# Optimization experiments

Hardware: AMD Instinct MI355X
Metric: run time of the kernel (lower is better)

Reference implementation:

```python
import jax, jax.numpy as jnp
import numpy as np

B, C, H, W = 256, 3, 128, 128
K = 16                      # vae_small.img_size == kernel == stride (non-overlapping)
GH, GW = H // K, W // K
P = C * K * K               # 768 flattened patch dim
HID = 2048
L = 256                     # latent_size


def setup_inputs() -> dict:
    key = jax.random.key(0)
    ks = jax.random.split(key, 9)
    s = 0.02
    f32 = jnp.float32
    return {
        "x": jax.random.uniform(ks[0], (B, C, H, W), f32),
        "w_enc1": jax.random.normal(ks[1], (P, HID), f32) * s,
        "b_enc1": jnp.zeros((HID,), f32),
        "w_enc2": jax.random.normal(ks[2], (HID, 2 * L), f32) * s,
        "b_enc2": jnp.zeros((2 * L,), f32),
        "w_dec1": jax.random.normal(ks[3], (L, HID), f32) * s,
        "b_dec1": jnp.zeros((HID,), f32),
        "w_dec2": jax.random.normal(ks[4], (HID, P), f32) * s,
        "b_dec2": jnp.zeros((P,), f32),
    }


def reference(x, w_enc1, b_enc1, w_enc2, b_enc2, w_dec1, b_dec1, w_dec2, b_dec2):
    b, c, h, w = x.shape
    gh, gw = h // K, w // K
    # unfold: [b,c,h,w] -> [b,gh,gw, c*K*K]  (same padding is 0 when stride==k)
    patches = (x.reshape(b, c, gh, K, gw, K)
                .transpose(0, 2, 4, 1, 3, 5)
                .reshape(b, gh, gw, c * K * K))
    # batched per-patch VAE encode (replaces the python map/unbind loop)
    he = jax.nn.relu(patches @ w_enc1 + b_enc1)            # [b,gh,gw,HID]
    mu_logvar = he @ w_enc2 + b_enc2                        # [b,gh,gw,2L]
    mu = mu_logvar[..., :L]
    z = mu                                                  # deterministic reparameterize
    # batched per-patch decode
    hd = jax.nn.relu(z @ w_dec1 + b_dec1)                   # [b,gh,gw,HID]
    dec = jax.nn.sigmoid(hd @ w_dec2 + b_dec2)              # [b,gh,gw,P]
    # fold: exact inverse of unfold since stride == kernel
    recon_x = (dec.reshape(b, gh, gw, c, K, K)
                 .transpose(0, 3, 1, 4, 2, 5)
                 .reshape(b, c, h, w))
    mu_logvar_2d = jnp.transpose(mu_logvar, (0, 3, 1, 2))   # [b, 2L, gh, gw]
    return recon_x, mu_logvar_2d
```

## Files before the change

### kernel.cpp

```cpp
#include <hip/hip_runtime.h>
#include <hip/hip_bf16.h>
#include <stdint.h>

typedef __bf16 bf16x8_t __attribute__((ext_vector_type(8)));
typedef float f32x4_t __attribute__((ext_vector_type(4)));
typedef unsigned short ushort8_t __attribute__((ext_vector_type(8)));

__device__ __forceinline__ unsigned short f2bf(float f) {
    union { float f; uint32_t i; } v; v.f = f;
    uint32_t i = v.i + (((v.i >> 16) & 1u) + 0x7FFFu);
    return (unsigned short)(i >> 16);
}

typedef const __attribute__((address_space(1))) void* gas_t;
typedef __attribute__((address_space(3))) void* las_t;
__device__ __forceinline__ void load_lds16(const unsigned short* g, unsigned short* l) {
    __builtin_amdgcn_global_load_lds((gas_t)g, (las_t)l, 16, 0, 0);
}

#define BB   256
#define CC   3
#define HH   128
#define WW   128
#define PP   768
#define HID  2048
#define LL   256
#define MM   16384

__global__ void patchify(const float* __restrict__ x,
                         unsigned short* __restrict__ patches) {
    int t = blockIdx.x * 256 + threadIdx.x;
    int e = t * 8;
    int col = e & 127;
    int row = (e >> 7) & 127;
    int c   = (e >> 14) % 3;
    int b   = e / (128 * 128 * 3);
    int gh = row >> 4, kh = row & 15, gw = col >> 4, kw = col & 15;
    long po = (long)(b * 64 + gh * 8 + gw) * PP + c * 256 + kh * 16 + kw;
    float4 v0 = *(const float4*)(x + e);
    float4 v1 = *(const float4*)(x + e + 4);
    ushort8_t o;
    o[0] = f2bf(v0.x); o[1] = f2bf(v0.y); o[2] = f2bf(v0.z); o[3] = f2bf(v0.w);
    o[4] = f2bf(v1.x); o[5] = f2bf(v1.y); o[6] = f2bf(v1.z); o[7] = f2bf(v1.w);
    *(ushort8_t*)(patches + po) = o;
}

__global__ void transpose_k(const float* __restrict__ in,
                            unsigned short* __restrict__ out, int R, int C) {
    __shared__ unsigned short tile[32][34];
    int nbc = C >> 5;
    int tc = blockIdx.x % nbc, tr = blockIdx.x / nbc;
    int tx = threadIdx.x & 31, ty0 = threadIdx.x >> 5;
    int r0 = tr << 5, c0 = tc << 5;
    #pragma unroll
    for (int i = 0; i < 4; ++i) {
        int ty = ty0 + i * 8;
        tile[ty][tx] = f2bf(in[(long)(r0 + ty) * C + c0 + tx]);
    }
    __syncthreads();
    #pragma unroll
    for (int i = 0; i < 4; ++i) {
        int ty = ty0 + i * 8;
        out[(long)(c0 + ty) * R + r0 + tx] = tile[tx][ty];
    }
}

#define BMT 256
#define BNT 128
#define BKT 32
#define LDS_TILE ((BMT + BNT) * BKT)

template <int ACT, int WMODE>
__global__ void __launch_bounds__(512, 4)
gemm_bt(const unsigned short* __restrict__ A, int lda,
        const unsigned short* __restrict__ Bt,
        const float* __restrict__ bias,
        unsigned short* __restrict__ C0u,
        float* __restrict__ C0f,
        float* __restrict__ C1f,
        int ldc, int Kd, int nbn, int m0) {
    __shared__ __align__(16) unsigned short lds_buf[3 * LDS_TILE];
    const int nbm = gridDim.x / nbn;
    const int stripe = nbm >> 3;
    const int xcd = blockIdx.x & 7;
    const int loc = blockIdx.x >> 3;
    const int bm = xcd * stripe + (loc % stripe);
    const int bn = loc / stripe;
    const int tid = threadIdx.x;
    const int wave = tid >> 6;
    const int lane = tid & 63;
    const int wr = wave >> 1;
    const int wc = wave & 1;
    const int fr = lane & 15;
    const int quad = lane >> 4;

    const int Gl = tid ^ ((tid >> 3) & 7);
    const int sr = Gl >> 2;
    const int sg = (Gl & 3) << 3;

    const unsigned short* Ab = A + (long)bm * BMT * lda;
    const unsigned short* Bb = Bt + (long)bn * BNT * Kd;

    int gA[4], gB[4];
    #pragma unroll
    for (int i = 0; i < 4; ++i) {
        const int r = (wr << 6) + (i << 4) + fr;
        gA[i] = ((((r << 2) | quad) ^ ((r >> 1) & 7)) << 3);
    }
    #pragma unroll
    for (int j = 0; j < 4; ++j) {
        const int r = (wc << 6) + (j << 4) + fr;
        gB[j] = ((((r << 2) | quad) ^ ((r >> 1) & 7)) << 3);
    }

    f32x4_t acc[4][4];
    #pragma unroll
    for (int i = 0; i < 4; ++i)
        #pragma unroll
        for (int j = 0; j < 4; ++j)
            acc[i][j] = (f32x4_t){0.f, 0.f, 0.f, 0.f};

    const int nt = Kd / BKT;

    #define STAGE(t, buf) do {                                                 \
        unsigned short* Al_ = (buf);                                           \
        unsigned short* Bl_ = Al_ + BMT * BKT;                                 \
        const long k0_ = (long)(t) * BKT;                                      \
        load_lds16(Ab + (long)sr * lda + k0_ + sg,         Al_ + (wave << 9)); \
        load_lds16(Ab + (long)(sr + 128) * lda + k0_ + sg,                     \
                   Al_ + 4096 + (wave << 9));                                  \
        load_lds16(Bb + (long)sr * Kd + k0_ + sg,          Bl_ + (wave << 9)); \
    } while (0)

    STAGE(0, lds_buf);
    STAGE(1, lds_buf + LDS_TILE);
    asm volatile("s_waitcnt vmcnt(3)" ::: "memory");
    __builtin_amdgcn_s_barrier();
    __builtin_amdgcn_sched_barrier(0);

    int rb = 0;
    int sbx = 2;
    for (int t = 0; t < nt; ++t) {
        if (t + 2 < nt) STAGE(t + 2, lds_buf + sbx * LDS_TILE);
        const unsigned short* Al = lds_buf + rb * LDS_TILE;
        const unsigned short* Bl = Al + BMT * BKT;
        bf16x8_t af[4], bfr[4];
        #pragma unroll
        for (int i = 0; i < 4; ++i) af[i] = *(const bf16x8_t*)&Al[gA[i]];
        #pragma unroll
        for (int j = 0; j < 4; ++j) bfr[j] = *(const bf16x8_t*)&Bl[gB[j]];
        __builtin_amdgcn_s_setprio(1);
        #pragma unroll
        for (int i = 0; i < 4; ++i)
            #pragma unroll
            for (int j = 0; j < 4; ++j)
                acc[i][j] = __builtin_amdgcn_mfma_f32_16x16x32_bf16(
                    af[i], bfr[j], acc[i][j], 0, 0, 0);
        __builtin_amdgcn_s_setprio(0);
        rb  = (rb == 2)  ? 0 : rb + 1;
        sbx = (sbx == 2) ? 0 : sbx + 1;
        if (t + 1 < nt) {
            if (t + 2 < nt) asm volatile("s_waitcnt vmcnt(3)" ::: "memory");
            else            asm volatile("s_waitcnt vmcnt(0)" ::: "memory");
            __builtin_amdgcn_s_barrier();
            __builtin_amdgcn_sched_barrier(0);
        }
    }
    #undef STAGE

    const int gcol0 = bn * BNT + (wc << 6);
    const int grow0 = bm * BMT + (wr << 6);
    #pragma unroll
    for (int j = 0; j < 4; ++j) {
        const int n = gcol0 + (j << 4) + fr;
        const float bv = bias[n];
        #pragma unroll
        for (int i = 0; i < 4; ++i) {
            #pragma unroll
            for (int r = 0; r < 4; ++r) {
                const int m = grow0 + (i << 4) + (quad << 2) + r;
                float v = acc[i][j][r] + bv;
                if (ACT == 1) v = fmaxf(v, 0.f);
                if (ACT == 2) v = 1.f / (1.f + __expf(-v));
                if (WMODE == 0) {
                    C0u[(long)m * ldc + n] = f2bf(v);
                } else if (WMODE == 1) {
                    const int gm = m0 + m;
                    C1f[((long)(gm >> 6) * 512 + n) * 64 + (gm & 63)] = v;
                    if (n < 256) C0u[(long)m * 256 + n] = f2bf(v);
                } else {
                    const int gm = m0 + m;
                    const int b = gm >> 6, g6 = gm & 63;
                    const int gh = g6 >> 3, gw = g6 & 7;
                    const int c = n >> 8, kh = (n >> 4) & 15, kw = n & 15;
                    const long o = (long)(b * 3 + c) * 16384
                                 + ((gh << 4) + kh) * 128 + (gw << 4) + kw;
                    C0f[o] = v;
                }
            }
        }
    }
}

extern "C" void kernel_launch(void* const* d_in, const int* in_sizes, int n_in,
                              void* d_out, int out_size, void* d_ws, size_t ws_size,
                              hipStream_t stream) {
    const float* x      = (const float*)d_in[0];
    const float* w_enc1 = (const float*)d_in[1];
    const float* b_enc1 = (const float*)d_in[2];
    const float* w_enc2 = (const float*)d_in[3];
    const float* b_enc2 = (const float*)d_in[4];
    const float* w_dec1 = (const float*)d_in[5];
    const float* b_dec1 = (const float*)d_in[6];
    const float* w_dec2 = (const float*)d_in[7];
    const float* b_dec2 = (const float*)d_in[8];
    float* outf = (float*)d_out;
    unsigned short* patches = (unsigned short*)d_out;
    float* out_ml = outf + (long)MM * PP;

    const size_t WT_ELEMS = 2048 * 768 + 512 * 2048 + 2048 * 256 + 768 * 2048;
    unsigned short* sb;
    long Mc;
    if (ws_size >= (WT_ELEMS + (size_t)MM * (LL + HID)) * 2) {
        sb = (unsigned short*)d_ws;  Mc = MM;
    } else {
        sb = (unsigned short*)d_in[0]; Mc = 8192;
    }
    unsigned short* wT1 = sb;
    unsigned short* wT2 = wT1 + 2048 * 768;
    unsigned short* wT3 = wT2 + 512 * 2048;
    unsigned short* wT4 = wT3 + 2048 * 256;
    unsigned short* mu  = wT4 + 768 * 2048;
    unsigned short* he  = mu + Mc * LL;

    patchify<<<6144, 256, 0, stream>>>(x, patches);

    transpose_k<<<(768 / 32) * (2048 / 32), 256, 0, stream>>>(w_enc1, wT1, 768, 2048);
    transpose_k<<<(2048 / 32) * (512 / 32), 256, 0, stream>>>(w_enc2, wT2, 2048, 512);
    transpose_k<<<(256 / 32) * (2048 / 32), 256, 0, stream>>>(w_dec1, wT3, 256, 2048);
    transpose_k<<<(2048 / 32) * (768 / 32), 256, 0, stream>>>(w_dec2, wT4, 2048, 768);

    const int nbm = (int)(Mc / BMT);
    for (long m0 = MM - Mc; m0 >= 0; m0 -= Mc) {
        gemm_bt<1, 0><<<nbm * (HID / BNT), 512, 0, stream>>>(
            patches + m0 * PP, PP, wT1, b_enc1,
            he, nullptr, nullptr, HID, PP, HID / BNT, 0);
        gemm_bt<0, 1><<<nbm * (512 / BNT), 512, 0, stream>>>(
            he, HID, wT2, b_enc2,
            mu, nullptr, out_ml, 0, HID, 512 / BNT, (int)m0);
        gemm_bt<1, 0><<<nbm * (HID / BNT), 512, 0, stream>>>(
            mu, LL, wT3, b_dec1,
            he, nullptr, nullptr, HID, LL, HID / BNT, 0);
        gemm_bt<2, 2><<<nbm * (PP / BNT), 512, 0, stream>>>(
            he, HID, wT4, b_dec2,
            nullptr, outf, nullptr, 0, HID, PP / BNT, (int)m0);
    }
}
```

Measured before the change: 375.7 us.

## Use 128x128-tile triple-buffered GEMM kernel for the narrow encoder-2 layer

Adds a second GEMM kernel with 128x128 tiles, 256 threads, three LDS stages and XCD-aware block mapping, and uses it only for the N=512 encoder-2 projection. The larger default tile gives too few blocks for this narrow GEMM, so smaller tiles are meant to raise block count and occupancy across CUs. In exchange each tile reuses its operands less and the code now carries a duplicated kernel.

```diff
diff --git a/kernel.cpp b/kernel.cpp
--- a/kernel.cpp
+++ b/kernel.cpp
@@ -202,6 +202,140 @@
     }
 }
 
+template <int ACT, int WMODE>
+__global__ void __launch_bounds__(256, 3)
+gemm_bt128(const unsigned short* __restrict__ A, int lda,
+           const unsigned short* __restrict__ Bt,
+           const float* __restrict__ bias,
+           unsigned short* __restrict__ C0u,
+           float* __restrict__ C0f,
+           float* __restrict__ C1f,
+           int ldc, int Kd, int nbn, int m0) {
+    __shared__ __align__(16) unsigned short lds_buf[3 * 8192];
+    const int nbm = gridDim.x / nbn;
+    const int stripe = nbm >> 3;
+    const int xcd = blockIdx.x & 7;
+    const int loc = blockIdx.x >> 3;
+    const int bm = xcd * stripe + (loc % stripe);
+    const int bn = loc / stripe;
+    const int tid = threadIdx.x;
+    const int wave = tid >> 6;
+    const int lane = tid & 63;
+    const int wr = wave >> 1;
+    const int wc = wave & 1;
+    const int fr = lane & 15;
+    const int quad = lane >> 4;
+
+    const int Gl = tid ^ ((tid >> 3) & 7);
+    const int sr = Gl >> 2;
+    const int sg = (Gl & 3) << 3;
+
+    const unsigned short* Ab = A + (long)bm * 128 * lda;
+    const unsigned short* Bb = Bt + (long)bn * 128 * Kd;
+
+    int gA[4], gB[4];
+    #pragma unroll
+    for (int i = 0; i < 4; ++i) {
+        const int r = (wr << 6) + (i << 4) + fr;
+        gA[i] = ((((r << 2) | quad) ^ ((r >> 1) & 7)) << 3);
+    }
+    #pragma unroll
+    for (int j = 0; j < 4; ++j) {
+        const int r = (wc << 6) + (j << 4) + fr;
+        gB[j] = ((((r << 2) | quad) ^ ((r >> 1) & 7)) << 3);
+    }
+
+    f32x4_t acc[4][4];
+    #pragma unroll
+    for (int i = 0; i < 4; ++i)
+        #pragma unroll
+        for (int j = 0; j < 4; ++j)
+            acc[i][j] = (f32x4_t){0.f, 0.f, 0.f, 0.f};
+
+    const int nt = Kd / 32;
+
+    #define STAGE128(t, buf) do {                                              \
+        unsigned short* Al_ = (buf);                                           \
+        unsigned short* Bl_ = Al_ + 4096;                                      \
+        const long k0_ = (long)(t) * 32;                                       \
+        load_lds16(Ab + (long)sr * lda + k0_ + sg,        Al_ + (wave << 9));  \
+        load_lds16(Ab + (long)(sr + 64) * lda + k0_ + sg,                      \
+                   Al_ + 2048 + (wave << 9));                                  \
+        load_lds16(Bb + (long)sr * Kd + k0_ + sg,         Bl_ + (wave << 9));  \
+        load_lds16(Bb + (long)(sr + 64) * Kd + k0_ + sg,                       \
+                   Bl_ + 2048 + (wave << 9));                                  \
+    } while (0)
+
+    STAGE128(0, lds_buf);
+    STAGE128(1, lds_buf + 8192);
+    asm volatile("s_waitcnt vmcnt(4)" ::: "memory");
+    __builtin_amdgcn_s_barrier();
+    __builtin_amdgcn_sched_barrier(0);
+
+    int rb = 0;
+    int sbx = 2;
+    for (int t = 0; t < nt; ++t) {
+        if (t + 2 < nt) STAGE128(t + 2, lds_buf + sbx * 8192);
+        const unsigned short* Al = lds_buf + rb * 8192;
+        const unsigned short* Bl = Al + 4096;
+        bf16x8_t af[4], bfr[4];
+        #pragma unroll
+        for (int i = 0; i < 4; ++i) af[i] = *(const bf16x8_t*)&Al[gA[i]];
+        #pragma unroll
+        for (int j = 0; j < 4; ++j) bfr[j] = *(const bf16x8_t*)&Bl[gB[j]];
+        __builtin_amdgcn_s_setprio(1);
+        #pragma unroll
+        for (int i = 0; i < 4; ++i)
+            #pragma unroll
+            for (int j = 0; j < 4; ++j)
+                acc[i][j] = __builtin_amdgcn_mfma_f32_16x16x32_bf16(
+                    af[i], bfr[j], acc[i][j], 0, 0, 0);
+        __builtin_amdgcn_s_setprio(0);
+        rb  = (rb == 2)  ? 0 : rb + 1;
+        sbx = (sbx == 2) ? 0 : sbx + 1;
+        if (t + 1 < nt) {
+            if (t + 2 < nt) asm volatile("s_waitcnt vmcnt(4)" ::: "memory");
+            else            asm volatile("s_waitcnt vmcnt(0)" ::: "memory");
+            __builtin_amdgcn_s_barrier();
+            __builtin_amdgcn_sched_barrier(0);
+        }
+    }
+    #undef STAGE128
+
+    const int gcol0 = bn * 128 + (wc << 6);
+    const int grow0 = bm * 128 + (wr << 6);
+    #pragma unroll
+    for (int j = 0; j < 4; ++j) {
+        const int n = gcol0 + (j << 4) + fr;
+        const float bv = bias[n];
+        #pragma unroll
+        for (int i = 0; i < 4; ++i) {
+            #pragma unroll
+            for (int r = 0; r < 4; ++r) {
+                const int m = grow0 + (i << 4) + (quad << 2) + r;
+                float v = acc[i][j][r] + bv;
+                if (ACT == 1) v = fmaxf(v, 0.f);
+                if (ACT == 2) v = 1.f / (1.f + __expf(-v));
+                if (WMODE == 0) {
+                    C0u[(long)m * ldc + n] = f2bf(v);
+                } else if (WMODE == 1) {
+                    const int gm = m0 + m;
+                    C1f[((long)(gm >> 6) * 512 + n) * 64 + (gm & 63)] = v;
+                    if (n < 256) C0u[(long)m * 256 + n] = f2bf(v);
+                } else {
+                    const int gm = m0 + m;
+                    const int b = gm >> 6, g6 = gm & 63;
+                    const int gh = g6 >> 3, gw = g6 & 7;
+                    const int c = n >> 8, kh = (n >> 4) & 15, kw = n & 15;
+                    const long o = (long)(b * 3 + c) * 16384
+                                 + ((gh << 4) + kh) * 128 + (gw << 4) + kw;
+                    C0f[o] = v;
+                }
+            }
+        }
+    }
+}
+
 extern "C" void kernel_launch(void* const* d_in, const int* in_sizes, int n_in,
                               void* d_out, int out_size, void* d_ws, size_t ws_size,
                               hipStream_t stream) {
@@ -245,9 +379,9 @@
         gemm_bt<1, 0><<<nbm * (HID / BNT), 512, 0, stream>>>(
             patches + m0 * PP, PP, wT1, b_enc1,
             he, nullptr, nullptr, HID, PP, HID / BNT, 0);
-        gemm_bt<0, 1><<<nbm * (512 / BNT), 512, 0, stream>>>(
+        gemm_bt128<0, 1><<<(int)(Mc / 128) * (512 / 128), 256, 0, stream>>>(
             he, HID, wT2, b_enc2,
-            mu, nullptr, out_ml, 0, HID, 512 / BNT, (int)m0);
+            mu, nullptr, out_ml, 0, HID, 512 / 128, (int)m0);
         gemm_bt<1, 0><<<nbm * (HID / BNT), 512, 0, stream>>>(
             mu, LL, wT3, b_dec1,
             he, nullptr, nullptr, HID, LL, HID / BNT, 0);
```

Result: faster. 349.3 us (-7.0%).
